# Kernel optimization log

Hardware: AMD Instinct MI355X
Metric: run time of the kernel (lower is better)

The kernel has to match this reference:

```python
import jax, jax.numpy as jnp
import numpy as np

B, N_Q, N_KV, D, H = 2, 2048, 2048, 512, 8
HD = D // H
NEG = -10000.0
LN_EPS = 1e-5


def setup_inputs() -> dict:
    key = jax.random.key(0)
    ks = jax.random.split(key, 8)
    s = 1.0 / np.sqrt(D)
    return {
        "query": jax.random.normal(ks[0], (B, N_Q, D), jnp.float32),
        "key_value": jax.random.normal(ks[1], (B, N_KV, D), jnp.float32),
        "Wq": jax.random.normal(ks[2], (D, D), jnp.float32) * s,
        "bq": jnp.zeros((D,), jnp.float32),
        "Wk": jax.random.normal(ks[3], (D, D), jnp.float32) * s,
        "bk": jnp.zeros((D,), jnp.float32),
        "Wv": jax.random.normal(ks[4], (D, D), jnp.float32) * s,
        "bv": jnp.zeros((D,), jnp.float32),
        "ln_gamma": jnp.ones((D,), jnp.float32),
        "ln_beta": jnp.zeros((D,), jnp.float32),
    }


def reference(query, key_value, Wq, bq, Wk, bk, Wv, bv, ln_gamma, ln_beta):
    # combined sequence [B, S, D], S = N_q + N_kv
    combined = jnp.concatenate([query, key_value], axis=1)
    Bt, S, _ = combined.shape
    n_q = query.shape[1]

    def heads(x, W, b):
        return (x @ W + b).reshape(Bt, S, H, HD)

    q = heads(combined, Wq, bq)  # [B,S,H,hd]
    k = heads(combined, Wk, bk)
    v = heads(combined, Wv, bv)

    scores = jnp.einsum("bqhd,bkhd->bhqk", q, k) / jnp.sqrt(
        jnp.asarray(HD, q.dtype)
    )
    # additive mask: -10000 on key columns < N_q for every query row
    key_mask = jnp.where(jnp.arange(S) < n_q, jnp.asarray(NEG, q.dtype), 0.0)
    probs = jax.nn.softmax(scores + key_mask[None, None, None, :], axis=-1)
    ctx = jnp.einsum("bhqk,bkhd->bqhd", probs, v).reshape(Bt, S, D)

    attended_q = ctx[:, :n_q, :]  # [B, N_q, D]
    resid = query + attended_q  # dropout is identity in eval
    mu = jnp.mean(resid, axis=-1, keepdims=True)
    var = jnp.var(resid, axis=-1, keepdims=True)
    out = (resid - mu) / jnp.sqrt(var + LN_EPS) * ln_gamma + ln_beta
    return out
```

## Files before the change

### kernel.cpp

```cpp
#include <hip/hip_runtime.h>
#include <stdint.h>

#define B_     2
#define NQ     2048
#define NKV    2048
#define D_     512
#define H_     8
#define HD     64
#define MROWS  4096
#define NSPLIT 2
#define SKEYS  (NKV / NSPLIT)

typedef unsigned short u16;
typedef __attribute__((ext_vector_type(4))) unsigned short u16x4;
typedef __attribute__((ext_vector_type(8))) unsigned short u16x8;
typedef __attribute__((ext_vector_type(8))) __bf16 bf16x8;
typedef __attribute__((ext_vector_type(4))) float f32x4;

__device__ __forceinline__ u16 f2bf(float f) {
  union { float f; unsigned int u; } v; v.f = f;
  unsigned int u = v.u;
  unsigned int r = (u + 0x7FFFu + ((u >> 16) & 1u)) >> 16;
  return (u16)r;
}
__device__ __forceinline__ float bf2f(u16 b) {
  union { unsigned int u; float f; } v; v.u = ((unsigned int)b) << 16;
  return v.f;
}
__device__ __forceinline__ unsigned cvtpk(float a, float b) {
  unsigned r;
  asm("v_cvt_pk_bf16_f32 %0, %1, %2" : "=v"(r) : "v"(a), "v"(b));
  return r;
}
__device__ __forceinline__ float exp2fast(float x) {
  return __builtin_amdgcn_exp2f(x);
}

__device__ __forceinline__ f32x4 mfma16(u16x8 a, u16x8 b, f32x4 c) {
  return __builtin_amdgcn_mfma_f32_16x16x32_bf16(
      __builtin_bit_cast(bf16x8, a), __builtin_bit_cast(bf16x8, b), c, 0, 0, 0);
}

#define QSCL 0.18033688011112042f

__global__ __launch_bounds__(256) void prep_kernel(
    const float* __restrict__ q, const float* __restrict__ kv,
    const float* __restrict__ Wq, const float* __restrict__ Wk,
    const float* __restrict__ Wv,
    u16* __restrict__ qb, u16* __restrict__ kvb,
    u16* __restrict__ wqt, u16* __restrict__ wkt, u16* __restrict__ wvt) {
  __shared__ float tile[32][33];
  int bx = blockIdx.x;
  if (bx < 2048) {
    int i = bx * 256 + threadIdx.x;
    float4 a = ((const float4*)q)[i];
    float4 b = ((const float4*)kv)[i];
    u16x4 ua = { f2bf(a.x), f2bf(a.y), f2bf(a.z), f2bf(a.w) };
    u16x4 ub = { f2bf(b.x), f2bf(b.y), f2bf(b.z), f2bf(b.w) };
    ((u16x4*)qb)[i]  = ua;
    ((u16x4*)kvb)[i] = ub;
  } else {
    int t = bx - 2048;
    int which = t >> 8;
    t &= 255;
    int tr = t >> 4, tc = t & 15;
    const float* W = (which == 0) ? Wq : (which == 1) ? Wk : Wv;
    u16* WT = (which == 0) ? wqt : (which == 1) ? wkt : wvt;

    int tx = threadIdx.x & 31, ty = threadIdx.x >> 5;
#pragma unroll
    for (int i = 0; i < 4; ++i)
      tile[ty + 8 * i][tx] = W[(size_t)(tr * 32 + ty + 8 * i) * D_ + tc * 32 + tx];
    __syncthreads();
#pragma unroll
    for (int i = 0; i < 4; ++i)
      WT[(size_t)(tc * 32 + ty + 8 * i) * D_ + tr * 32 + tx] =
          f2bf(tile[tx][ty + 8 * i]);
  }
}

__global__ __launch_bounds__(64) void gemm_qkv(
    const u16* __restrict__ qb, const u16* __restrict__ kvb,
    const u16* __restrict__ wqt, const u16* __restrict__ wkt,
    const u16* __restrict__ wvt,
    const float* __restrict__ bq, const float* __restrict__ bk,
    const float* __restrict__ bv,
    u16* __restrict__ Qp, u16* __restrict__ Kp, u16* __restrict__ VpT) {
  __shared__ __align__(16) u16 tile[64][72];

  int lane = threadIdx.x;
  int cl = lane & 15, g = lane >> 4;
  int y = blockIdx.y;
  int which = y >> 3;
  int col0 = (y & 7) * 64;
  int row0 = blockIdx.x * 64;

  const u16* A   = (which == 0) ? qb : kvb;
  const u16* WT  = (which == 0) ? wqt : (which == 1) ? wkt : wvt;
  const float* bias = (which == 0) ? bq : (which == 1) ? bk : bv;
  u16* Out = (which == 0) ? Qp : (which == 1) ? Kp : VpT;
  float oscale = (which == 0) ? QSCL : 1.0f;

  const u16* Abase = A  + (size_t)(row0 + cl) * D_ + g * 8;
  const u16* Bbase = WT + (size_t)(col0 + cl) * D_ + g * 8;

  f32x4 acc[4][4] = {};
  u16x8 afA[4], bfA[4], afB[4], bfB[4];
#pragma unroll
  for (int i = 0; i < 4; ++i) afA[i] = *(const u16x8*)(Abase + (size_t)i * 16 * D_);
#pragma unroll
  for (int j = 0; j < 4; ++j) bfA[j] = *(const u16x8*)(Bbase + (size_t)j * 16 * D_);

#pragma unroll
  for (int kk = 0; kk < 16; ++kk) {
    const u16x8* ca = (kk & 1) ? afB : afA;
    const u16x8* cw = (kk & 1) ? bfB : bfA;
    u16x8* na = (kk & 1) ? afA : afB;
    u16x8* nw = (kk & 1) ? bfA : bfB;
    if (kk < 15) {
      int k0 = kk * 32 + 32;
#pragma unroll
      for (int i = 0; i < 4; ++i) na[i] = *(const u16x8*)(Abase + (size_t)i * 16 * D_ + k0);
#pragma unroll
      for (int j = 0; j < 4; ++j) nw[j] = *(const u16x8*)(Bbase + (size_t)j * 16 * D_ + k0);
    }
    __builtin_amdgcn_s_setprio(1);
#pragma unroll
    for (int i = 0; i < 4; ++i)
#pragma unroll
      for (int j = 0; j < 4; ++j)
        acc[i][j] = mfma16(ca[i], cw[j], acc[i][j]);
    __builtin_amdgcn_s_setprio(0);
  }

#pragma unroll
  for (int j = 0; j < 4; ++j) {
    float bv2 = bias[col0 + j * 16 + cl];
#pragma unroll
    for (int i = 0; i < 4; ++i)
#pragma unroll
      for (int r = 0; r < 4; ++r) {
        u16 val = f2bf((acc[i][j][r] + bv2) * oscale);
        int rr = i * 16 + g * 4 + r, cc = j * 16 + cl;
        if (which != 2) tile[rr][cc] = val;
        else            tile[cc][rr] = val;
      }
  }
  u16* dst;
  if (which != 2) {
    dst = Out + (size_t)(row0 + lane) * D_ + col0;
  } else {
    int b_ = row0 >> 11, key0 = row0 & (NKV - 1);
    dst = Out + (size_t)b_ * (D_ * NKV) + (size_t)(col0 + lane) * NKV + key0;
  }
#pragma unroll
  for (int c8 = 0; c8 < 8; ++c8) {
    uint4 v = *(const uint4*)&tile[lane][c8 * 8];
    *(uint4*)(dst + c8 * 8) = v;
  }
}

__global__ __launch_bounds__(64, 2) void attn_kernel(
    const u16* __restrict__ Q, const u16* __restrict__ K,
    const u16* __restrict__ VpT, u16* __restrict__ opart,
    float* __restrict__ ml) {
  __shared__ union __align__(16) {
    u16 p[64][66];
    unsigned t[64][33];
  } sm;

  int lane = threadIdx.x;
  int cl = lane & 15, g = lane >> 4;

  int lin = blockIdx.x;
  int xcd = lin & 7, k_ = lin >> 3;
  int bhHi = k_ >> 6;
  int r_ = k_ & 63;
  int bh = xcd + 8 * bhHi;
  int q0 = (r_ >> 1) * 64;
  int s  = r_ & 1;
  int b = bh >> 3, h = bh & 7;

  u16x8 qf[4][2];
  {
    const u16* Qb = Q + ((size_t)(b * NQ + q0 + cl)) * D_ + h * HD + g * 8;
#pragma unroll
    for (int f = 0; f < 4; ++f)
#pragma unroll
      for (int kk = 0; kk < 2; ++kk)
        qf[f][kk] = *(const u16x8*)(Qb + (size_t)f * 16 * D_ + kk * 32);
  }

  const u16* kptr[4];
  const u16* vptr[4];
#pragma unroll
  for (int kf_ = 0; kf_ < 4; ++kf_)
    kptr[kf_] = K + ((size_t)b * NKV + s * SKEYS + kf_ * 16 + cl) * D_ + h * HD + g * 8;
#pragma unroll
  for (int j = 0; j < 4; ++j)
    vptr[j] = VpT + (size_t)b * (D_ * NKV) + (size_t)(h * HD + j * 16 + cl) * NKV
                  + s * SKEYS + g * 8;

  f32x4 o[4][4] = {};
  float lsum[4] = { 0.f, 0.f, 0.f, 0.f };

  const int NT = SKEYS / 64;

  for (int t = 0; t < NT; ++t) {
    u16x8 kf[4][2];
#pragma unroll
    for (int kf_ = 0; kf_ < 4; ++kf_)
#pragma unroll
      for (int kk = 0; kk < 2; ++kk)
        kf[kf_][kk] = *(const u16x8*)(kptr[kf_] + kk * 32);

    f32x4 sa[4][4] = {};
    __builtin_amdgcn_s_setprio(1);
#pragma unroll
    for (int kk = 0; kk < 2; ++kk)
#pragma unroll
      for (int kf_ = 0; kf_ < 4; ++kf_)
#pragma unroll
        for (int f = 0; f < 4; ++f)
          sa[kf_][f] = mfma16(kf[kf_][kk], qf[f][kk], sa[kf_][f]);
    __builtin_amdgcn_s_setprio(0);

    u16x8 vf[4][2];
#pragma unroll
    for (int j = 0; j < 4; ++j)
#pragma unroll
      for (int kk = 0; kk < 2; ++kk)
        vf[j][kk] = *(const u16x8*)(vptr[j] + kk * 32);

#pragma unroll
    for (int f = 0; f < 4; ++f) {
      float ps = 0.f;
#pragma unroll
      for (int kf_ = 0; kf_ < 4; ++kf_)
#pragma unroll
        for (int r = 0; r < 4; ++r) {
          float p = exp2fast(sa[kf_][f][r]);
          sa[kf_][f][r] = p;
          ps += p;
        }
      lsum[f] += ps;
    }

#pragma unroll
    for (int f = 0; f < 4; ++f)
#pragma unroll
      for (int kf_ = 0; kf_ < 4; ++kf_) {
        unsigned lo = cvtpk(sa[kf_][f][0], sa[kf_][f][1]);
        unsigned hi = cvtpk(sa[kf_][f][2], sa[kf_][f][3]);
        unsigned* P32 = (unsigned*)&sm.p[f * 16 + cl][kf_ * 16 + g * 4];
        P32[0] = lo;
        P32[1] = hi;
      }

#pragma unroll
    for (int kk = 0; kk < 2; ++kk) {
      __builtin_amdgcn_s_setprio(1);
#pragma unroll
      for (int f = 0; f < 4; ++f) {
        u16x8 pa = *(const u16x8*)&sm.p[f * 16 + cl][kk * 32 + g * 8];
#pragma unroll
        for (int j = 0; j < 4; ++j)
          o[f][j] = mfma16(vf[j][kk], pa, o[f][j]);
      }
      __builtin_amdgcn_s_setprio(0);
    }

#pragma unroll
    for (int kf_ = 0; kf_ < 4; ++kf_) kptr[kf_] += 64 * D_;
#pragma unroll
    for (int j = 0; j < 4; ++j) vptr[j] += 64;
  }

#pragma unroll
  for (int f = 0; f < 4; ++f) {
    lsum[f] += __shfl_xor(lsum[f], 16, 64);
    lsum[f] += __shfl_xor(lsum[f], 32, 64);
  }

#pragma unroll
  for (int f = 0; f < 4; ++f)
#pragma unroll
    for (int j = 0; j < 4; ++j) {
      int row = f * 16 + cl;
      sm.t[row][j * 8 + g * 2 + 0] = cvtpk(o[f][j][0], o[f][j][1]);
      sm.t[row][j * 8 + g * 2 + 1] = cvtpk(o[f][j][2], o[f][j][3]);
    }
  if (g == 0) {
#pragma unroll
    for (int f = 0; f < 4; ++f) {
      size_t mi = ((size_t)(bh * NSPLIT + s) * NQ + q0 + f * 16 + cl) * 2;
      ml[mi]     = 0.f;
      ml[mi + 1] = lsum[f];
    }
  }
  __syncthreads();
  {
    int row = lane;
    u16* op = opart + (size_t)(bh * NSPLIT + s) * NQ * HD + (size_t)(q0 + row) * HD;
#pragma unroll
    for (int i = 0; i < 8; ++i) {
      uint4 v;
      v.x = sm.t[row][i * 4 + 0];
      v.y = sm.t[row][i * 4 + 1];
      v.z = sm.t[row][i * 4 + 2];
      v.w = sm.t[row][i * 4 + 3];
      *(uint4*)(op + i * 8) = v;
    }
  }
}

__global__ __launch_bounds__(256) void combine_ln_kernel(
    const float* __restrict__ query, const u16* __restrict__ opart,
    const float* __restrict__ ml,
    const float* __restrict__ gamma, const float* __restrict__ beta,
    float* __restrict__ out) {
  int row = blockIdx.x * 4 + (threadIdx.x >> 6);
  int lane = threadIdx.x & 63;
  int b = row >> 11, q = row & (NQ - 1);
  int h = lane >> 3;

  float ms[NSPLIT], ls[NSPLIT];
  float mmax = -1e30f;
#pragma unroll
  for (int s = 0; s < NSPLIT; ++s) {
    size_t mi = ((size_t)((b * H_ + h) * NSPLIT + s) * NQ + q) * 2;
    ms[s] = ml[mi];
    ls[s] = ml[mi + 1];
    mmax = fmaxf(mmax, ms[s]);
  }
  float lt = 0.f;
#pragma unroll
  for (int s = 0; s < NSPLIT; ++s) lt += ls[s] * exp2fast(ms[s] - mmax);
  float inv = 1.f / lt;

  size_t base = (size_t)row * D_;
  const float4* q4 = (const float4*)(query + base);
  float4 a0 = q4[lane * 2], a1 = q4[lane * 2 + 1];
  float x[8] = { a0.x, a0.y, a0.z, a0.w, a1.x, a1.y, a1.z, a1.w };

#pragma unroll
  for (int s = 0; s < NSPLIT; ++s) {
    size_t oi = ((size_t)((b * H_ + h) * NSPLIT + s) * NQ + q) * HD + (lane & 7) * 8;
    u16x8 ov = *(const u16x8*)(opart + oi);
    float sc = exp2fast(ms[s] - mmax) * inv;
#pragma unroll
    for (int e = 0; e < 8; ++e) x[e] += bf2f(ov[e]) * sc;
  }

  float sum = 0.f, sq = 0.f;
#pragma unroll
  for (int e = 0; e < 8; ++e) { sum += x[e]; sq += x[e] * x[e]; }
#pragma unroll
  for (int d = 1; d < 64; d <<= 1) {
    sum += __shfl_xor(sum, d, 64);
    sq  += __shfl_xor(sq,  d, 64);
  }
  float mean = sum * (1.f / D_);
  float var  = sq * (1.f / D_) - mean * mean;
  float rstd = rsqrtf(var + 1e-5f);

  const float4* g4  = (const float4*)gamma;
  const float4* be4 = (const float4*)beta;
  float4 g0 = g4[lane * 2], g1 = g4[lane * 2 + 1];
  float4 e0 = be4[lane * 2], e1 = be4[lane * 2 + 1];
  float4 o0, o1;
  o0.x = (x[0] - mean) * rstd * g0.x + e0.x;
  o0.y = (x[1] - mean) * rstd * g0.y + e0.y;
  o0.z = (x[2] - mean) * rstd * g0.z + e0.z;
  o0.w = (x[3] - mean) * rstd * g0.w + e0.w;
  o1.x = (x[4] - mean) * rstd * g1.x + e1.x;
  o1.y = (x[5] - mean) * rstd * g1.y + e1.y;
  o1.z = (x[6] - mean) * rstd * g1.z + e1.z;
  o1.w = (x[7] - mean) * rstd * g1.w + e1.w;
  ((float4*)(out + base))[lane * 2]     = o0;
  ((float4*)(out + base))[lane * 2 + 1] = o1;
}

extern "C" void kernel_launch(void* const* d_in, const int* in_sizes, int n_in,
                              void* d_out, int out_size, void* d_ws, size_t ws_size,
                              hipStream_t stream) {
  const float* query     = (const float*)d_in[0];
  const float* key_value = (const float*)d_in[1];
  const float* Wq = (const float*)d_in[2];
  const float* bq = (const float*)d_in[3];
  const float* Wk = (const float*)d_in[4];
  const float* bk = (const float*)d_in[5];
  const float* Wv = (const float*)d_in[6];
  const float* bv = (const float*)d_in[7];
  const float* gamma = (const float*)d_in[8];
  const float* beta  = (const float*)d_in[9];
  float* out = (float*)d_out;

  char* ws = (char*)d_ws;
  u16* Qp    = (u16*)(ws + 0);
  u16* Kp    = (u16*)(ws + 4194304);
  u16* VpT   = (u16*)(ws + 8388608);
  u16* opart = (u16*)(ws + 12582912);
  float* ml  = (float*)(ws + 29360128);
  u16* qb    = (u16*)(ws + 12582912);
  u16* kvb   = (u16*)(ws + 16777216);
  u16* wqt   = (u16*)(ws + 20971520);
  u16* wkt   = (u16*)(ws + 21495808);
  u16* wvt   = (u16*)(ws + 22020096);

  prep_kernel<<<2816, 256, 0, stream>>>(query, key_value, Wq, Wk, Wv,
                                        qb, kvb, wqt, wkt, wvt);
  dim3 gg(MROWS / 64, 24);
  gemm_qkv<<<gg, 64, 0, stream>>>(qb, kvb, wqt, wkt, wvt, bq, bk, bv,
                                  Qp, Kp, VpT);
  attn_kernel<<<1024, 64, 0, stream>>>(Qp, Kp, VpT, opart, ml);
  combine_ln_kernel<<<MROWS / 4, 256, 0, stream>>>(query, opart, ml, gamma, beta, out);
}
```

Baseline: 82.83 us.

## Drop split-KV attention and normalize context inside attention kernel

```diff
diff --git a/kernel.cpp b/kernel.cpp
--- a/kernel.cpp
+++ b/kernel.cpp
@@ -8,8 +8,6 @@
 #define H_     8
 #define HD     64
 #define MROWS  4096
-#define NSPLIT 2
-#define SKEYS  (NKV / NSPLIT)
 
 typedef unsigned short u16;
 typedef __attribute__((ext_vector_type(4))) unsigned short u16x4;
@@ -162,8 +160,7 @@
 
 __global__ __launch_bounds__(64, 2) void attn_kernel(
     const u16* __restrict__ Q, const u16* __restrict__ K,
-    const u16* __restrict__ VpT, u16* __restrict__ opart,
-    float* __restrict__ ml) {
+    const u16* __restrict__ VpT, u16* __restrict__ octx) {
   __shared__ union __align__(16) {
     u16 p[64][66];
     unsigned t[64][33];
@@ -174,11 +171,10 @@
 
   int lin = blockIdx.x;
   int xcd = lin & 7, k_ = lin >> 3;
-  int bhHi = k_ >> 6;
-  int r_ = k_ & 63;
+  int bhHi = k_ >> 5;
+  int r_ = k_ & 31;
   int bh = xcd + 8 * bhHi;
-  int q0 = (r_ >> 1) * 64;
-  int s  = r_ & 1;
+  int q0 = r_ * 64;
   int b = bh >> 3, h = bh & 7;
 
   u16x8 qf[4][2];
@@ -195,16 +191,16 @@
   const u16* vptr[4];
 #pragma unroll
   for (int kf_ = 0; kf_ < 4; ++kf_)
-    kptr[kf_] = K + ((size_t)b * NKV + s * SKEYS + kf_ * 16 + cl) * D_ + h * HD + g * 8;
+    kptr[kf_] = K + ((size_t)b * NKV + kf_ * 16 + cl) * D_ + h * HD + g * 8;
 #pragma unroll
   for (int j = 0; j < 4; ++j)
     vptr[j] = VpT + (size_t)b * (D_ * NKV) + (size_t)(h * HD + j * 16 + cl) * NKV
-                  + s * SKEYS + g * 8;
+                  + g * 8;
 
   f32x4 o[4][4] = {};
   float lsum[4] = { 0.f, 0.f, 0.f, 0.f };
 
-  const int NT = SKEYS / 64;
+  const int NT = NKV / 64;
 
   for (int t = 0; t < NT; ++t) {
     u16x8 kf[4][2];
@@ -276,10 +272,12 @@
     for (int j = 0; j < 4; ++j) vptr[j] += 64;
   }
 
+  float inv[4];
 #pragma unroll
   for (int f = 0; f < 4; ++f) {
     lsum[f] += __shfl_xor(lsum[f], 16, 64);
     lsum[f] += __shfl_xor(lsum[f], 32, 64);
+    inv[f] = 1.f / lsum[f];
   }
 
 #pragma unroll
@@ -287,21 +285,13 @@
 #pragma unroll
     for (int j = 0; j < 4; ++j) {
       int row = f * 16 + cl;
-      sm.t[row][j * 8 + g * 2 + 0] = cvtpk(o[f][j][0], o[f][j][1]);
-      sm.t[row][j * 8 + g * 2 + 1] = cvtpk(o[f][j][2], o[f][j][3]);
-    }
-  if (g == 0) {
-#pragma unroll
-    for (int f = 0; f < 4; ++f) {
-      size_t mi = ((size_t)(bh * NSPLIT + s) * NQ + q0 + f * 16 + cl) * 2;
-      ml[mi]     = 0.f;
-      ml[mi + 1] = lsum[f];
-    }
-  }
+      sm.t[row][j * 8 + g * 2 + 0] = cvtpk(o[f][j][0] * inv[f], o[f][j][1] * inv[f]);
+      sm.t[row][j * 8 + g * 2 + 1] = cvtpk(o[f][j][2] * inv[f], o[f][j][3] * inv[f]);
+    }
   __syncthreads();
   {
     int row = lane;
-    u16* op = opart + (size_t)(bh * NSPLIT + s) * NQ * HD + (size_t)(q0 + row) * HD;
+    u16* op = octx + (size_t)bh * NQ * HD + (size_t)(q0 + row) * HD;
 #pragma unroll
     for (int i = 0; i < 8; ++i) {
       uint4 v;
@@ -314,9 +304,8 @@
   }
 }
 
-__global__ __launch_bounds__(256) void combine_ln_kernel(
-    const float* __restrict__ query, const u16* __restrict__ opart,
-    const float* __restrict__ ml,
+__global__ __launch_bounds__(256) void resid_ln_kernel(
+    const float* __restrict__ query, const u16* __restrict__ octx,
     const float* __restrict__ gamma, const float* __restrict__ beta,
     float* __restrict__ out) {
   int row = blockIdx.x * 4 + (threadIdx.x >> 6);
@@ -324,32 +313,16 @@
   int b = row >> 11, q = row & (NQ - 1);
   int h = lane >> 3;
 
-  float ms[NSPLIT], ls[NSPLIT];
-  float mmax = -1e30f;
-#pragma unroll
-  for (int s = 0; s < NSPLIT; ++s) {
-    size_t mi = ((size_t)((b * H_ + h) * NSPLIT + s) * NQ + q) * 2;
-    ms[s] = ml[mi];
-    ls[s] = ml[mi + 1];
-    mmax = fmaxf(mmax, ms[s]);
-  }
-  float lt = 0.f;
-#pragma unroll
-  for (int s = 0; s < NSPLIT; ++s) lt += ls[s] * exp2fast(ms[s] - mmax);
-  float inv = 1.f / lt;
-
   size_t base = (size_t)row * D_;
   const float4* q4 = (const float4*)(query + base);
   float4 a0 = q4[lane * 2], a1 = q4[lane * 2 + 1];
   float x[8] = { a0.x, a0.y, a0.z, a0.w, a1.x, a1.y, a1.z, a1.w };
 
-#pragma unroll
-  for (int s = 0; s < NSPLIT; ++s) {
-    size_t oi = ((size_t)((b * H_ + h) * NSPLIT + s) * NQ + q) * HD + (lane & 7) * 8;
-    u16x8 ov = *(const u16x8*)(opart + oi);
-    float sc = exp2fast(ms[s] - mmax) * inv;
-#pragma unroll
-    for (int e = 0; e < 8; ++e) x[e] += bf2f(ov[e]) * sc;
+  {
+    size_t oi = ((size_t)(b * H_ + h) * NQ + q) * HD + (lane & 7) * 8;
+    u16x8 ov = *(const u16x8*)(octx + oi);
+#pragma unroll
+    for (int e = 0; e < 8; ++e) x[e] += bf2f(ov[e]);
   }
 
   float sum = 0.f, sq = 0.f;
@@ -400,8 +373,7 @@
   u16* Qp    = (u16*)(ws + 0);
   u16* Kp    = (u16*)(ws + 4194304);
   u16* VpT   = (u16*)(ws + 8388608);
-  u16* opart = (u16*)(ws + 12582912);
-  float* ml  = (float*)(ws + 29360128);
+  u16* octx  = (u16*)(ws + 12582912);
   u16* qb    = (u16*)(ws + 12582912);
   u16* kvb   = (u16*)(ws + 16777216);
   u16* wqt   = (u16*)(ws + 20971520);
@@ -413,6 +385,6 @@
   dim3 gg(MROWS / 64, 24);
   gemm_qkv<<<gg, 64, 0, stream>>>(qb, kvb, wqt, wkt, wvt, bq, bk, bv,
                                   Qp, Kp, VpT);
-  attn_kernel<<<1024, 64, 0, stream>>>(Qp, Kp, VpT, opart, ml);
-  combine_ln_kernel<<<MROWS / 4, 256, 0, stream>>>(query, opart, ml, gamma, beta, out);
-}
+  attn_kernel<<<512, 64, 0, stream>>>(Qp, Kp, VpT, octx);
+  resid_ln_kernel<<<MROWS / 4, 256, 0, stream>>>(query, octx, gamma, beta, out);
+}
```

After: 99.43 us. 20.0% more time.
